# Performance work log

Measured on AMD Instinct MI355X. Metric: run time of the kernel, lower is better.

The kernel has to match this reference:

```python
import jax, jax.numpy as jnp
import numpy as np
from jax import lax

N = 4096        # num graph nodes
T = 8           # timesteps (LSTM batch dim in original, batch_first=False)
IN_DIM = 64
H = 128         # hidden_dim
OUT_DIM = 1
E_RAND = 65536  # random edges; self-loops appended -> E = 69632


def setup_inputs() -> dict:
    key = jax.random.key(0)
    ks = jax.random.split(key, 18)
    s = 0.05
    f = lambda k, shp: (jax.random.normal(k, shp, jnp.float32) * s)
    src = jnp.concatenate([jax.random.randint(ks[15], (E_RAND,), 0, N), jnp.arange(N)]).astype(jnp.int32)
    dst = jnp.concatenate([jax.random.randint(ks[16], (E_RAND,), 0, N), jnp.arange(N)]).astype(jnp.int32)
    return {
        "input": jax.random.normal(ks[0], (N, T, IN_DIM), jnp.float32),
        "hidden": f(ks[1], (1, T, H)),
        "cell": f(ks[2], (1, T, H)),
        "pre_w": f(ks[3], (IN_DIM, H)),
        "pre_b": f(ks[4], (H,)),
        "w_ih": f(ks[5], (4 * H, H)),
        "w_hh": f(ks[6], (4 * H, H)),
        "b_ih": f(ks[7], (4 * H,)),
        "b_hh": f(ks[8], (4 * H,)),
        "gat_wsrc": f(ks[9], (H, H)),
        "gat_wdst": f(ks[10], (H, H)),
        "gat_attn": f(ks[11], (H,)),
        "gat_b": f(ks[12], (H,)),
        "out_w": f(ks[13], (H, OUT_DIM)),
        "out_b": f(ks[14], (OUT_DIM,)),
        "edge_src": src,
        "edge_dst": dst,
    }


def reference(input, hidden, cell, pre_w, pre_b, w_ih, w_hh, b_ih, b_hh,
              gat_wsrc, gat_wdst, gat_attn, gat_b, out_w, out_b,
              edge_src, edge_dst):
    n_nodes = input.shape[0]
    x = input @ pre_w + pre_b                         # (N, T, H)
    b = b_ih + b_hh

    # LSTM over node dimension (seq = nodes); the T per-timestep runs of the
    # original Python loop are independent (init states come from the given
    # hidden/cell), so we batch them along T.
    def step(carry, x_n):                             # x_n: (T, H)
        h, c = carry
        g = x_n @ w_ih.T + h @ w_hh.T + b             # (T, 4H), torch gate order i,f,g,o
        i_g, f_g, g_g, o_g = jnp.split(g, 4, axis=-1)
        c = jax.nn.sigmoid(f_g) * c + jax.nn.sigmoid(i_g) * jnp.tanh(g_g)
        h = jax.nn.sigmoid(o_g) * jnp.tanh(c)
        return (h, c), h

    (hT, cT), outs = lax.scan(step, (hidden[0], cell[0]), x)   # outs: (N, T, H)

    # GATv2Conv (DGL semantics, num_heads=1, share_weights=False)
    fs = outs @ gat_wsrc                              # (N, T, H)
    fd = outs @ gat_wdst
    e = jax.nn.leaky_relu(fs[edge_src] + fd[edge_dst], 0.2)    # (E, T, H)
    logits = e @ gat_attn                             # (E, T)
    # edge softmax per destination node (numerically stable)
    m = lax.stop_gradient(jax.ops.segment_max(logits, edge_dst, num_segments=n_nodes))
    a = jnp.exp(logits - m[edge_dst])
    denom = jax.ops.segment_sum(a, edge_dst, num_segments=n_nodes)
    alpha = a / denom[edge_dst]                       # (E, T)
    agg = jax.ops.segment_sum(alpha[..., None] * fs[edge_src], edge_dst, num_segments=n_nodes)
    rst = agg + gat_b                                 # (N, T, H)

    # dropout is identity in eval mode
    y = rst @ out_w + out_b                           # (N, T, OUT_DIM)
    return (y, hT[None], cT[None])
```

## Files before the change

kernel.cpp:

```cpp
#include <hip/hip_runtime.h>
#include <hip/hip_bf16.h>

#define N_NODES 4096
#define T_STEPS 8
#define INDIM   64
#define HDIM    128
#define G4      512
#define NROWS   (N_NODES * T_STEPS)
#define LOG2E   1.4426950408889634f

typedef __hip_bfloat16 bf16;
typedef __attribute__((ext_vector_type(8))) short bf16x8;
typedef __attribute__((ext_vector_type(4))) float f32x4;
typedef __attribute__((ext_vector_type(8))) int   i32x8;

__device__ __forceinline__ float asfloat_u(unsigned int u) {
    union { unsigned int i; float f; } v; v.i = u; return v.f;
}
__device__ __forceinline__ float fexp2(float x) {
    float r; asm("v_exp_f32 %0, %1" : "=v"(r) : "v"(x)); return r;
}

#define P_O0 32768
#define P_O1 (P_O0 + 512)
#define P_O2 (P_O1 + 16384)
#define P_O3 (P_O2 + 16384)
#define P_O4 (P_O3 + 128)
#define P_O5 (P_O4 + 1)
#define P_O6 (P_O5 + 65536)
#define P_O7 (P_O6 + 128)
__global__ void prep_kernel(const float* __restrict__ pre_w, const float* __restrict__ pre_b,
                            const float* __restrict__ w_ih, const float* __restrict__ b_ih,
                            const float* __restrict__ b_hh, const float* __restrict__ w_hh,
                            const float* __restrict__ wsrc, const float* __restrict__ wdst,
                            const float* __restrict__ out_w, const float* __restrict__ out_b,
                            const float* __restrict__ gat_b, const float* __restrict__ attn,
                            float* __restrict__ Wc, float* __restrict__ bc,
                            float* __restrict__ wsT, float* __restrict__ wdT,
                            float* __restrict__ wso, float* __restrict__ cy,
                            unsigned char* __restrict__ whh8, float* __restrict__ attn2) {
    int id = blockIdx.x * 256 + threadIdx.x;
    if (id < P_O0) {
        int g = id >> 6, i = id & 63;
        float s = 0.f;
        for (int k = 0; k < HDIM; k++) s += pre_w[i * HDIM + k] * w_ih[g * HDIM + k];
        int gate = g >> 7;
        Wc[id] = s * ((gate == 2) ? -2.f * LOG2E : -LOG2E);
    } else if (id < P_O1) {
        int g = id - P_O0;
        float s = b_ih[g] + b_hh[g];
        for (int k = 0; k < HDIM; k++) s += pre_b[k] * w_ih[g * HDIM + k];
        int gate = g >> 7;
        bc[g] = s * ((gate == 2) ? -2.f * LOG2E : -LOG2E);
    } else if (id < P_O2) {
        int c = id - P_O1;
        int co = c >> 7, k = c & 127;
        wsT[c] = wsrc[k * HDIM + co];
    } else if (id < P_O3) {
        int c = id - P_O2;
        int co = c >> 7, k = c & 127;
        wdT[c] = wdst[k * HDIM + co];
    } else if (id < P_O4) {
        int hi = id - P_O3;
        float s = 0.f;
        for (int ho = 0; ho < HDIM; ho++) s += wsrc[hi * HDIM + ho] * out_w[ho];
        wso[hi] = s;
    } else if (id == P_O4) {
        float s = out_b[0];
        for (int h = 0; h < HDIM; h++) s += gat_b[h] * out_w[h];
        cy[0] = s;
    } else if (id < P_O6) {
        int c = id - P_O5;
        int gate = c >> 14;
        float v = w_hh[c] * ((gate == 2) ? -2.f * LOG2E : -LOG2E);
        int pk = __builtin_amdgcn_cvt_pk_fp8_f32(v, v, 0, false);
        whh8[c] = (unsigned char)(pk & 0xff);
    } else if (id < P_O7) {
        int c = id - P_O6;
        attn2[c] = attn[c] * LOG2E;
    }
}

__global__ __launch_bounds__(512) void xw_kernel(const float* __restrict__ input,
                                                 const float* __restrict__ Wc,
                                                 const float* __restrict__ bc,
                                                 bf16* __restrict__ xw) {
    __shared__ __align__(16) float in_lds[16 * INDIM];
    int tid = threadIdx.x;
    int rowbase = blockIdx.x * 16;
    in_lds[tid]       = input[(size_t)rowbase * INDIM + tid];
    in_lds[tid + 512] = input[(size_t)rowbase * INDIM + tid + 512];
    __syncthreads();
    int g = tid;
    int gate = g >> 7, hh = g & 127;
    float4 w[16];
    const float4* wr = reinterpret_cast<const float4*>(Wc + g * INDIM);
#pragma unroll
    for (int u = 0; u < 16; u++) w[u] = wr[u];
    float b = bc[g];
    for (int r = 0; r < 16; r++) {
        const float4* hv = reinterpret_cast<const float4*>(in_lds + r * INDIM);
        float a0 = b, a1 = 0.f, a2 = 0.f, a3 = 0.f;
#pragma unroll
        for (int u = 0; u < 16; u++) {
            float4 h4 = hv[u]; float4 wv = w[u];
            a0 = fmaf(h4.x, wv.x, a0); a1 = fmaf(h4.y, wv.y, a1);
            a2 = fmaf(h4.z, wv.z, a2); a3 = fmaf(h4.w, wv.w, a3);
        }
        xw[(size_t)(rowbase + r) * G4 + hh * 4 + gate] = __float2bfloat16((a0 + a1) + (a2 + a3));
    }
}

__global__ void hist_kernel(const int* __restrict__ edst, int nE, int* __restrict__ cnt) {
    int i = blockIdx.x * 256 + threadIdx.x;
    if (i < nE) atomicAdd(&cnt[edst[i]], 1);
}

__global__ __launch_bounds__(512) void scan_kernel(const int* __restrict__ cnt,
                                                   int* __restrict__ rowptr) {
    __shared__ int part[512];
    int t = threadIdx.x, base = t * 8;
    int loc[8]; int s = 0;
#pragma unroll
    for (int j = 0; j < 8; j++) { loc[j] = s; s += cnt[base + j]; }
    part[t] = s;
    __syncthreads();
    for (int off = 1; off < 512; off <<= 1) {
        int v = (t >= off) ? part[t - off] : 0;
        __syncthreads();
        part[t] += v;
        __syncthreads();
    }
    int pre = part[t] - s;
#pragma unroll
    for (int j = 0; j < 8; j++) rowptr[base + j] = pre + loc[j];
    if (t == 511) rowptr[4096] = part[511];
}

__global__ void scatter_kernel(const int* __restrict__ esrc, const int* __restrict__ edst,
                               int nE, const int* __restrict__ rowptr,
                               int* __restrict__ cnt2, int* __restrict__ ssrc) {
    int i = blockIdx.x * 256 + threadIdx.x;
    if (i < nE) {
        int d = edst[i];
        int pos = rowptr[d] + atomicAdd(&cnt2[d], 1);
        ssrc[pos] = esrc[i];
    }
}

__global__ __launch_bounds__(512, 1) void lstm_kernel(const bf16* __restrict__ xw,
                                                      const unsigned char* __restrict__ whh8,
                                                      const float* __restrict__ hidden0,
                                                      const float* __restrict__ cell0,
                                                      float* __restrict__ outs,
                                                      float* __restrict__ dout) {
    __shared__ __align__(16) char hbuf0[4 * 144];
    __shared__ __align__(16) char hbuf1[4 * 144];
    const int tid  = threadIdx.x;
    const int w    = tid >> 6;
    const int lane = tid & 63;
    const int kg   = lane >> 4;
    const int lr   = lane & 15;
    const int q    = lr & 3;
    const int d    = lr >> 2;
    const int qg   = blockIdx.x * 4 + q;
    const int hb   = 16 * w + kg * 4 + d;

    i32x8 afr[4];
#pragma unroll
    for (int G = 0; G < 4; G++) {
        const unsigned char* rowp = whh8 + (size_t)(G * 128 + 16 * w + lr) * HDIM + kg * 32;
        afr[G] = *reinterpret_cast<const i32x8*>(rowp);
    }

    const int roff = q * 144 + kg * 32;
    const int woff = q * 144 + hb;
    const int sc   = 0x7f7f7f7f;

    float cv = cell0[qg * HDIM + hb];
    float hv = hidden0[qg * HDIM + hb];
    {
        int pk = __builtin_amdgcn_cvt_pk_fp8_f32(hv, hv, 0, false);
        *reinterpret_cast<unsigned char*>(hbuf0 + woff) = (unsigned char)(pk & 0xff);
    }

    const uint2* xq = reinterpret_cast<const uint2*>(xw) + qg * 128 + hb;
    float* outp = outs + qg * HDIM + hb;

    uint2 xb[8];
#pragma unroll
    for (int i = 0; i < 8; i++) xb[i] = xq[i * 1024];
    __syncthreads();

#define STEPX(NIDX, RB, WB, XQ)                                                      \
    do {                                                                             \
        i32x8 bfr = *reinterpret_cast<const i32x8*>(RB + roff);                      \
        f32x4 z = {0.f, 0.f, 0.f, 0.f};                                              \
        f32x4 acc0 = __builtin_amdgcn_mfma_scale_f32_16x16x128_f8f6f4(               \
            afr[0], bfr, z, 0, 0, 0, sc, 0, sc);                                     \
        f32x4 acc1 = __builtin_amdgcn_mfma_scale_f32_16x16x128_f8f6f4(               \
            afr[1], bfr, z, 0, 0, 0, sc, 0, sc);                                     \
        f32x4 acc2 = __builtin_amdgcn_mfma_scale_f32_16x16x128_f8f6f4(               \
            afr[2], bfr, z, 0, 0, 0, sc, 0, sc);                                     \
        f32x4 acc3 = __builtin_amdgcn_mfma_scale_f32_16x16x128_f8f6f4(               \
            afr[3], bfr, z, 0, 0, 0, sc, 0, sc);                                     \
        float s0 = (d & 2) ? ((d & 1) ? acc0[3] : acc0[2])                           \
                           : ((d & 1) ? acc0[1] : acc0[0]);                          \
        float s1 = (d & 2) ? ((d & 1) ? acc1[3] : acc1[2])                           \
                           : ((d & 1) ? acc1[1] : acc1[0]);                          \
        float s2 = (d & 2) ? ((d & 1) ? acc2[3] : acc2[2])                           \
                           : ((d & 1) ? acc2[1] : acc2[0]);                          \
        float s3 = (d & 2) ? ((d & 1) ? acc3[3] : acc3[2])                           \
                           : ((d & 1) ? acc3[1] : acc3[0]);                          \
        float gi = s0 + asfloat_u((XQ).x << 16);                                     \
        float gf = s1 + asfloat_u((XQ).x & 0xffff0000u);                             \
        float gg = s2 + asfloat_u((XQ).y << 16);                                     \
        float go = s3 + asfloat_u((XQ).y & 0xffff0000u);                             \
        float A = fexp2(gi), C = fexp2(gf), B = fexp2(gg);                           \
        float p = 1.f + A, r = 1.f + B, s = 1.f + C;                                 \
        float pr = p * r;                                                            \
        float num = fmaf(cv, pr, (2.f - r) * s);                                     \
        cv = num * __builtin_amdgcn_rcpf(pr * s);                                    \
        float O = fexp2(go), F = fexp2(cv * (-2.f * LOG2E));                         \
        float po = 1.f + O, rf = 1.f + F;                                            \
        hv = (2.f - rf) * __builtin_amdgcn_rcpf(po * rf);                            \
        int pk = __builtin_amdgcn_cvt_pk_fp8_f32(hv, hv, 0, false);                  \
        *reinterpret_cast<unsigned char*>(WB + woff) = (unsigned char)(pk & 0xff);   \
        outp[(NIDX) * 1024] = hv;                                                    \
        asm volatile("s_waitcnt lgkmcnt(0)" ::: "memory");                           \
        __builtin_amdgcn_s_barrier();                                                \
        __builtin_amdgcn_sched_barrier(0);                                           \
    } while (0)

    for (int n = 0; n < N_NODES; n += 8) {
#pragma unroll
        for (int i = 0; i < 8; i++) {
            if (i & 1) STEPX(n + i, hbuf1, hbuf0, xb[i]);
            else       STEPX(n + i, hbuf0, hbuf1, xb[i]);
            xb[i] = xq[(n + i + 8) * 1024];
        }
    }
#undef STEPX

    dout[NROWS + qg * HDIM + hb] = hv;
    dout[NROWS + T_STEPS * HDIM + qg * HDIM + hb] = cv;
}

__global__ __launch_bounds__(256) void fsfd_kernel(const float* __restrict__ outs,
                                                   const float* __restrict__ wsT,
                                                   const float* __restrict__ wdT,
                                                   const float* __restrict__ wso,
                                                   bf16* __restrict__ fs,
                                                   bf16* __restrict__ fd,
                                                   float* __restrict__ fso) {
    __shared__ __align__(16) float rows[32 * HDIM];
    int tid = threadIdx.x;
    size_t base = (size_t)blockIdx.x * 32 * HDIM;
#pragma unroll
    for (int j = 0; j < 16; j++) rows[tid + j * 256] = outs[base + tid + j * 256];
    __syncthreads();
    int c = tid;
    const float4* wT = reinterpret_cast<const float4*>(
        (c < HDIM) ? (wsT + c * HDIM) : (wdT + (c - HDIM) * HDIM));
    float4 w[32];
#pragma unroll
    for (int u = 0; u < 32; u++) w[u] = wT[u];
    bf16* dst = (c < HDIM) ? (fs + base + c) : (fd + base + (c - HDIM));
    for (int r = 0; r < 32; r++) {
        const float4* hv = reinterpret_cast<const float4*>(rows + r * HDIM);
        float a0 = 0.f, a1 = 0.f, a2 = 0.f, a3 = 0.f;
#pragma unroll
        for (int u = 0; u < 32; u++) {
            float4 h4 = hv[u]; float4 wv = w[u];
            a0 = fmaf(h4.x, wv.x, a0); a1 = fmaf(h4.y, wv.y, a1);
            a2 = fmaf(h4.z, wv.z, a2); a3 = fmaf(h4.w, wv.w, a3);
        }
        dst[(size_t)r * HDIM] = __float2bfloat16((a0 + a1) + (a2 + a3));
    }
    if (tid < 32) {
        const float* rp = rows + tid * HDIM;
        float s = 0.f;
        for (int k = 0; k < HDIM; k++) {
            int kk = (k + tid) & 127;
            s += rp[kk] * wso[kk];
        }
        fso[blockIdx.x * 32 + tid] = s;
    }
}

__global__ __launch_bounds__(64) void edge_csr_kernel(const int* __restrict__ ssrc,
                                                      const int* __restrict__ rowptr,
                                                      const bf16* __restrict__ fs,
                                                      const bf16* __restrict__ fd,
                                                      const float* __restrict__ attn2,
                                                      const float* __restrict__ fso,
                                                      const float* __restrict__ cy,
                                                      float* __restrict__ dout) {
    int dn = blockIdx.x;
    int l  = threadIdx.x;
    float a0 = attn2[2 * l], a1 = attn2[2 * l + 1];
    const unsigned int* fdp = reinterpret_cast<const unsigned int*>(fd) + (size_t)dn * 512 + l;
    unsigned int fdw[8];
#pragma unroll
    for (int t = 0; t < 8; t++) fdw[t] = fdp[t * 64];
    float den[8], num[8];
#pragma unroll
    for (int t = 0; t < 8; t++) { den[t] = 0.f; num[t] = 0.f; }
    int e0 = rowptr[dn], e1 = rowptr[dn + 1];
    for (int e = e0; e < e1; e++) {
        int s = ssrc[e];
        const unsigned int* fsp = reinterpret_cast<const unsigned int*>(fs) + (size_t)s * 512 + l;
        float4 fsoA = *reinterpret_cast<const float4*>(fso + s * 8);
        float4 fsoB = *reinterpret_cast<const float4*>(fso + s * 8 + 4);
        float fsov[8] = {fsoA.x, fsoA.y, fsoA.z, fsoA.w, fsoB.x, fsoB.y, fsoB.z, fsoB.w};
#pragma unroll
        for (int t = 0; t < 8; t++) {
            unsigned int uf = fsp[t * 64];
            float x1 = asfloat_u(uf << 16) + asfloat_u(fdw[t] << 16);
            float x2 = asfloat_u(uf & 0xffff0000u) + asfloat_u(fdw[t] & 0xffff0000u);
            x1 = fmaxf(x1, 0.f) + 0.2f * fminf(x1, 0.f);
            x2 = fmaxf(x2, 0.f) + 0.2f * fminf(x2, 0.f);
            float v = x1 * a0 + x2 * a1;
#pragma unroll
            for (int m = 32; m >= 1; m >>= 1) v += __shfl_xor(v, m, 64);
            float a = fexp2(v);
            den[t] += a;
            num[t] = fmaf(a, fsov[t], num[t]);
        }
    }
    if (l == 0) {
        float cyv = cy[0];
        float4 y0, y1;
        y0.x = num[0] * __builtin_amdgcn_rcpf(den[0]) + cyv;
        y0.y = num[1] * __builtin_amdgcn_rcpf(den[1]) + cyv;
        y0.z = num[2] * __builtin_amdgcn_rcpf(den[2]) + cyv;
        y0.w = num[3] * __builtin_amdgcn_rcpf(den[3]) + cyv;
        y1.x = num[4] * __builtin_amdgcn_rcpf(den[4]) + cyv;
        y1.y = num[5] * __builtin_amdgcn_rcpf(den[5]) + cyv;
        y1.z = num[6] * __builtin_amdgcn_rcpf(den[6]) + cyv;
        y1.w = num[7] * __builtin_amdgcn_rcpf(den[7]) + cyv;
        *reinterpret_cast<float4*>(dout + dn * 8)     = y0;
        *reinterpret_cast<float4*>(dout + dn * 8 + 4) = y1;
    }
}

extern "C" void kernel_launch(void* const* d_in, const int* in_sizes, int n_in,
                              void* d_out, int out_size, void* d_ws, size_t ws_size,
                              hipStream_t stream) {
    const float* input  = (const float*)d_in[0];
    const float* hidden = (const float*)d_in[1];
    const float* cell   = (const float*)d_in[2];
    const float* pre_w  = (const float*)d_in[3];
    const float* pre_b  = (const float*)d_in[4];
    const float* w_ih   = (const float*)d_in[5];
    const float* w_hh   = (const float*)d_in[6];
    const float* b_ih   = (const float*)d_in[7];
    const float* b_hh   = (const float*)d_in[8];
    const float* wsrc   = (const float*)d_in[9];
    const float* wdst   = (const float*)d_in[10];
    const float* attn   = (const float*)d_in[11];
    const float* gatb   = (const float*)d_in[12];
    const float* outw   = (const float*)d_in[13];
    const float* outb   = (const float*)d_in[14];
    const int*   esrc   = (const int*)d_in[15];
    const int*   edst   = (const int*)d_in[16];
    int nE = in_sizes[15];
    float* dout = (float*)d_out;
    char* ws = (char*)d_ws;

    const size_t o_xw    = 0;
    const size_t o_outs  = 33554432;
    const size_t o_fs    = 50331648;
    const size_t o_fd    = 58720256;
    const size_t o_fso   = 67108864;
    const size_t o_cnt   = 67239936;
    const size_t o_cnt2  = 67256320;
    const size_t o_rowptr= 67272704;
    const size_t o_ssrc  = 67289344;
    const size_t o_wc    = 67502080;
    const size_t o_bc    = 67633152;
    const size_t o_wsT   = 67635200;
    const size_t o_wdT   = 67700736;
    const size_t o_wso   = 67766272;
    const size_t o_cy    = 67766784;
    const size_t o_attn2 = 67767040;
    const size_t o_whh8  = o_fs;

    bf16*  xw    = (bf16*)(ws + o_xw);
    float* outs  = (float*)(ws + o_outs);
    bf16*  fs    = (bf16*)(ws + o_fs);
    bf16*  fd    = (bf16*)(ws + o_fd);
    float* fso   = (float*)(ws + o_fso);
    int*   cnt   = (int*)(ws + o_cnt);
    int*   cnt2  = (int*)(ws + o_cnt2);
    int*   rowptr= (int*)(ws + o_rowptr);
    int*   ssrc  = (int*)(ws + o_ssrc);
    float* Wc    = (float*)(ws + o_wc);
    float* bc    = (float*)(ws + o_bc);
    float* wsT   = (float*)(ws + o_wsT);
    float* wdT   = (float*)(ws + o_wdT);
    float* wso   = (float*)(ws + o_wso);
    float* cy    = (float*)(ws + o_cy);
    float* attn2 = (float*)(ws + o_attn2);
    unsigned char* whh8 = (unsigned char*)(ws + o_whh8);

    prep_kernel<<<516, 256, 0, stream>>>(pre_w, pre_b, w_ih, b_ih, b_hh, w_hh, wsrc, wdst,
                                         outw, outb, gatb, attn,
                                         Wc, bc, wsT, wdT, wso, cy, whh8, attn2);
    xw_kernel<<<2048, 512, 0, stream>>>(input, Wc, bc, xw);
    hipMemsetAsync(ws + o_cnt, 0, 32768, stream);
    hist_kernel<<<(nE + 255) / 256, 256, 0, stream>>>(edst, nE, cnt);
    scan_kernel<<<1, 512, 0, stream>>>(cnt, rowptr);
    scatter_kernel<<<(nE + 255) / 256, 256, 0, stream>>>(esrc, edst, nE, rowptr, cnt2, ssrc);
    lstm_kernel<<<2, 512, 0, stream>>>(xw, whh8, hidden, cell, outs, dout);
    fsfd_kernel<<<1024, 256, 0, stream>>>(outs, wsT, wdT, wso, fs, fd, fso);
    edge_csr_kernel<<<N_NODES, 64, 0, stream>>>(ssrc, rowptr, fs, fd, attn2, fso, cy, dout);
}
```

Measured before the change: 1.685 ms.

## Build CSR inside a spare LSTM block and pack four nodes per edge block

The separate memset, histogram, scan and scatter launches are removed. A third block of the sequential LSTM kernel now builds the CSR using shared-memory counters, overlapping that graph preprocessing with the latency-bound recurrence. The edge kernel also handles four destination nodes per 256-thread block instead of one per 64-thread block, cutting block count. The extra block adds a large shared array to every LSTM block, and the order of edges within each destination segment stays nondeterministic.

```diff
diff --git a/kernel.cpp b/kernel.cpp
--- a/kernel.cpp
+++ b/kernel.cpp
@@ -111,52 +111,55 @@
     }
 }
 
-__global__ void hist_kernel(const int* __restrict__ edst, int nE, int* __restrict__ cnt) {
-    int i = blockIdx.x * 256 + threadIdx.x;
-    if (i < nE) atomicAdd(&cnt[edst[i]], 1);
-}
-
-__global__ __launch_bounds__(512) void scan_kernel(const int* __restrict__ cnt,
-                                                   int* __restrict__ rowptr) {
-    __shared__ int part[512];
-    int t = threadIdx.x, base = t * 8;
-    int loc[8]; int s = 0;
-#pragma unroll
-    for (int j = 0; j < 8; j++) { loc[j] = s; s += cnt[base + j]; }
-    part[t] = s;
-    __syncthreads();
-    for (int off = 1; off < 512; off <<= 1) {
-        int v = (t >= off) ? part[t - off] : 0;
-        __syncthreads();
-        part[t] += v;
-        __syncthreads();
-    }
-    int pre = part[t] - s;
-#pragma unroll
-    for (int j = 0; j < 8; j++) rowptr[base + j] = pre + loc[j];
-    if (t == 511) rowptr[4096] = part[511];
-}
-
-__global__ void scatter_kernel(const int* __restrict__ esrc, const int* __restrict__ edst,
-                               int nE, const int* __restrict__ rowptr,
-                               int* __restrict__ cnt2, int* __restrict__ ssrc) {
-    int i = blockIdx.x * 256 + threadIdx.x;
-    if (i < nE) {
-        int d = edst[i];
-        int pos = rowptr[d] + atomicAdd(&cnt2[d], 1);
-        ssrc[pos] = esrc[i];
-    }
-}
-
 __global__ __launch_bounds__(512, 1) void lstm_kernel(const bf16* __restrict__ xw,
                                                       const unsigned char* __restrict__ whh8,
                                                       const float* __restrict__ hidden0,
                                                       const float* __restrict__ cell0,
                                                       float* __restrict__ outs,
-                                                      float* __restrict__ dout) {
+                                                      float* __restrict__ dout,
+                                                      const int* __restrict__ esrc,
+                                                      const int* __restrict__ edst,
+                                                      int nE,
+                                                      int* __restrict__ rowptr,
+                                                      int* __restrict__ ssrc) {
     __shared__ __align__(16) char hbuf0[4 * 144];
     __shared__ __align__(16) char hbuf1[4 * 144];
+    __shared__ int cnt[N_NODES];
+    __shared__ int part[512];
     const int tid  = threadIdx.x;
+
+    if (blockIdx.x == 2) {
+        for (int i = tid; i < N_NODES; i += 512) cnt[i] = 0;
+        __syncthreads();
+        for (int i = tid; i < nE; i += 512) atomicAdd(&cnt[edst[i]], 1);
+        __syncthreads();
+        int base = tid * 8, loc[8], s = 0;
+#pragma unroll
+        for (int j = 0; j < 8; j++) { loc[j] = s; s += cnt[base + j]; }
+        part[tid] = s;
+        __syncthreads();
+        for (int off = 1; off < 512; off <<= 1) {
+            int v = (tid >= off) ? part[tid - off] : 0;
+            __syncthreads();
+            part[tid] += v;
+            __syncthreads();
+        }
+        int pre = part[tid] - s;
+#pragma unroll
+        for (int j = 0; j < 8; j++) rowptr[base + j] = pre + loc[j];
+        if (tid == 511) rowptr[N_NODES] = nE;
+        __syncthreads();
+#pragma unroll
+        for (int j = 0; j < 8; j++) cnt[base + j] = pre + loc[j];
+        __syncthreads();
+        for (int i = tid; i < nE; i += 512) {
+            int d = edst[i];
+            int pos = atomicAdd(&cnt[d], 1);
+            ssrc[pos] = esrc[i];
+        }
+        return;
+    }
+
     const int w    = tid >> 6;
     const int lane = tid & 63;
     const int kg   = lane >> 4;
@@ -288,16 +291,16 @@
     }
 }
 
-__global__ __launch_bounds__(64) void edge_csr_kernel(const int* __restrict__ ssrc,
-                                                      const int* __restrict__ rowptr,
-                                                      const bf16* __restrict__ fs,
-                                                      const bf16* __restrict__ fd,
-                                                      const float* __restrict__ attn2,
-                                                      const float* __restrict__ fso,
-                                                      const float* __restrict__ cy,
-                                                      float* __restrict__ dout) {
-    int dn = blockIdx.x;
-    int l  = threadIdx.x;
+__global__ __launch_bounds__(256) void edge_csr_kernel(const int* __restrict__ ssrc,
+                                                       const int* __restrict__ rowptr,
+                                                       const bf16* __restrict__ fs,
+                                                       const bf16* __restrict__ fd,
+                                                       const float* __restrict__ attn2,
+                                                       const float* __restrict__ fso,
+                                                       const float* __restrict__ cy,
+                                                       float* __restrict__ dout) {
+    int dn = blockIdx.x * 4 + (threadIdx.x >> 6);
+    int l  = threadIdx.x & 63;
     float a0 = attn2[2 * l], a1 = attn2[2 * l + 1];
     const unsigned int* fdp = reinterpret_cast<const unsigned int*>(fd) + (size_t)dn * 512 + l;
     unsigned int fdw[8];
@@ -373,8 +376,6 @@
     const size_t o_fs    = 50331648;
     const size_t o_fd    = 58720256;
     const size_t o_fso   = 67108864;
-    const size_t o_cnt   = 67239936;
-    const size_t o_cnt2  = 67256320;
     const size_t o_rowptr= 67272704;
     const size_t o_ssrc  = 67289344;
     const size_t o_wc    = 67502080;
@@ -391,8 +392,6 @@
     bf16*  fs    = (bf16*)(ws + o_fs);
     bf16*  fd    = (bf16*)(ws + o_fd);
     float* fso   = (float*)(ws + o_fso);
-    int*   cnt   = (int*)(ws + o_cnt);
-    int*   cnt2  = (int*)(ws + o_cnt2);
     int*   rowptr= (int*)(ws + o_rowptr);
     int*   ssrc  = (int*)(ws + o_ssrc);
     float* Wc    = (float*)(ws + o_wc);
@@ -408,11 +407,8 @@
                                          outw, outb, gatb, attn,
                                          Wc, bc, wsT, wdT, wso, cy, whh8, attn2);
     xw_kernel<<<2048, 512, 0, stream>>>(input, Wc, bc, xw);
-    hipMemsetAsync(ws + o_cnt, 0, 32768, stream);
-    hist_kernel<<<(nE + 255) / 256, 256, 0, stream>>>(edst, nE, cnt);
-    scan_kernel<<<1, 512, 0, stream>>>(cnt, rowptr);
-    scatter_kernel<<<(nE + 255) / 256, 256, 0, stream>>>(esrc, edst, nE, rowptr, cnt2, ssrc);
-    lstm_kernel<<<2, 512, 0, stream>>>(xw, whh8, hidden, cell, outs, dout);
+    lstm_kernel<<<3, 512, 0, stream>>>(xw, whh8, hidden, cell, outs, dout,
+                                       esrc, edst, nE, rowptr, ssrc);
     fsfd_kernel<<<1024, 256, 0, stream>>>(outs, wsT, wdT, wso, fs, fd, fso);
-    edge_csr_kernel<<<N_NODES, 64, 0, stream>>>(ssrc, rowptr, fs, fd, attn2, fso, cy, dout);
-}
+    edge_csr_kernel<<<N_NODES / 4, 256, 0, stream>>>(ssrc, rowptr, fs, fd, attn2, fso, cy, dout);
+}
```

Result: no change. 1.660 ms (-1.5%).
